# Kernel tuning notes

Hardware: AMD Instinct MI355X
Metric: run time of the kernel (lower is better)

## Reference

```python
import jax, jax.numpy as jnp
import numpy as np

NEG_INF = -1e30  # fp32-safe sentinel for masked max


def setup_inputs() -> dict:
    key = jax.random.key(0)
    ks = jax.random.split(key, 8)
    E = 65536          # num_edge
    S = 1              # neg_samples
    D = 200            # dim_in_time + dim_in_node
    H = 100            # hardcoded hidden width of src_fc/dst_fc
    T = 8              # num edge types
    C = 1              # predict_class
    scale = 1.0 / np.sqrt(D)
    return {
        "h": jax.random.normal(ks[0], (E * (S + 2), D), dtype=jnp.float32),
        "src_W": jax.random.normal(ks[1], (T, D, H), dtype=jnp.float32) * scale,
        "src_b": jax.random.normal(ks[2], (T, H), dtype=jnp.float32) * 0.01,
        "dst_W": jax.random.normal(ks[3], (T, D, H), dtype=jnp.float32) * scale,
        "dst_b": jax.random.normal(ks[4], (T, H), dtype=jnp.float32) * 0.01,
        "out_W": jax.random.normal(ks[5], (T, H, C), dtype=jnp.float32) * (1.0 / np.sqrt(H)),
        "out_b": jax.random.normal(ks[6], (T, C), dtype=jnp.float32) * 0.01,
        "poss_edgetypes": jax.random.randint(ks[7], (E * (1 + S), T), 0, 2, dtype=jnp.int32),
        "neg_samples": S,
    }


def _masked_max_pred(h_s, h_d, mask, src_W, src_b, dst_W, dst_b, out_W, out_b):
    # h_s, h_d: [N, D]; mask: [N, T] bool
    src_enc = jnp.einsum('nd,tdh->nth', h_s, src_W) + src_b      # [N, T, H]
    dst_enc = jnp.einsum('nd,tdh->nth', h_d, dst_W) + dst_b      # [N, T, H]
    hid = jax.nn.relu(src_enc + dst_enc)                          # [N, T, H]
    pred = jnp.einsum('nth,thc->ntc', hid, out_W) + out_b        # [N, T, C]
    masked = jnp.where(mask[:, :, None], pred, NEG_INF)
    best = jnp.max(masked, axis=1)                                # [N, C]
    any_valid = jnp.any(mask, axis=1, keepdims=True)
    return jnp.where(any_valid, best, 0.0)                        # zeros if no valid type


def reference(h, src_W, src_b, dst_W, dst_b, out_W, out_b, poss_edgetypes, neg_samples):
    E = h.shape[0] // (neg_samples + 2)
    h_src = h[:E]
    h_pos_dst = h[E:2 * E]
    h_neg_dst = h[2 * E:]                                         # [S*E, D], neg-major order
    mask = poss_edgetypes.astype(bool)
    pos_mask = mask[:E]
    neg_mask = mask[E:]
    pos_pred = _masked_max_pred(h_src, h_pos_dst, pos_mask,
                                src_W, src_b, dst_W, dst_b, out_W, out_b)
    h_src_tiled = jnp.tile(h_src, (neg_samples, 1))               # matches global_neg_idx = src + neg*E
    neg_pred = _masked_max_pred(h_src_tiled, h_neg_dst, neg_mask,
                                src_W, src_b, dst_W, dst_b, out_W, out_b)
    return pos_pred, neg_pred
```

## Files before the change

kernel.cpp:

```cpp
#include <hip/hip_runtime.h>
#include <stdint.h>


typedef float f32x4 __attribute__((ext_vector_type(4)));
typedef short s16x8 __attribute__((ext_vector_type(8)));

static constexpr int E_NODES = 65536;
static constexpr int D_DIM   = 200;
static constexpr int H_DIM   = 100;
static constexpr int T_TYPES = 8;
static constexpr int NPAD    = 112;
static constexpr int NT      = 7;
static constexpr int KS      = 13;
static constexpr int BK      = 128;
static constexpr int SLPT    = 4;
static constexpr int P_TILE  = 128;
static constexpr int THREADS = 256;
static constexpr int N_INT   = T_TYPES * SLPT;
static constexpr int SLAB_ELEMS = NPAD * BK;
static constexpr int XFERS_PT   = SLAB_ELEMS * 2 / 16 / THREADS;

__device__ unsigned short g_Wt[N_INT * SLAB_ELEMS];

__device__ __forceinline__ unsigned short f2bf(float f) {
  unsigned int u = __float_as_uint(f);
  u += 0x7FFFu + ((u >> 16) & 1u);
  return (unsigned short)(u >> 16);
}

__global__ void prep_weights(const float* __restrict__ srcW, const float* __restrict__ dstW) {
  int idx = blockIdx.x * blockDim.x + threadIdx.x;
  const int total = N_INT * SLAB_ELEMS;
  if (idx >= total) return;
  int j   = idx % NPAD;
  int rem = idx / NPAD;
  int kk  = rem % BK;
  int rs  = rem / BK;
  int sl  = rs & 3;
  int t   = rs >> 2;
  int k   = sl * BK + kk;
  float v = 0.0f;
  if (j < H_DIM) {
    if (k < D_DIM)            v = srcW[(t * D_DIM + k) * H_DIM + j];
    else if (k < 2 * D_DIM)   v = dstW[(t * D_DIM + (k - D_DIM)) * H_DIM + j];
  }
  int kks = kk ^ ((j & 7) << 3);
  g_Wt[(rs * NPAD + j) * BK + kks] = f2bf(v);
}

__device__ __forceinline__ void stage(int rs, unsigned short* dst, int tid) {
  const char* src = (const char*)g_Wt + (size_t)rs * SLAB_ELEMS * 2;
  char* d = (char*)dst;
#pragma unroll
  for (int i = 0; i < XFERS_PT; ++i) {
    const int off = (i * THREADS + tid) * 16;
    __builtin_amdgcn_global_load_lds(
        (const __attribute__((address_space(1))) void*)(src + off),
        (__attribute__((address_space(3))) void*)(d + off),
        16, 0, 0);
  }
}

__global__ __launch_bounds__(THREADS, 2)
void fused_pred(const float* __restrict__ h,
                const float* __restrict__ srcB, const float* __restrict__ dstB,
                const float* __restrict__ outW, const float* __restrict__ outB,
                const int* __restrict__ poss, float* __restrict__ out) {
  __shared__ __align__(16) unsigned short ldsB[2][SLAB_ELEMS];
  __shared__ __align__(16) int   ldsMask[P_TILE * T_TYPES];
  __shared__ float ldsBias[T_TYPES * NPAD];
  __shared__ float ldsOutw[T_TYPES * NPAD];
  __shared__ float ldsOutb[T_TYPES];

  const int tid  = threadIdx.x;
  const int lane = tid & 63;
  const int w    = tid >> 6;
  const int c    = lane & 15;
  const int g    = lane >> 4;

  const int l     = ((int)blockIdx.x & 7) * 128 + ((int)blockIdx.x >> 3);
  const int which = l & 1;
  const int grp   = l >> 1;
  const int P0    = which * E_NODES + grp * P_TILE;

  stage(0, ldsB[0], tid);
  __builtin_amdgcn_sched_barrier(0);

#pragma unroll
  for (int i = 0; i < 4; ++i) {
    int idx = i * THREADS + tid;
    if (idx < T_TYPES * NPAD) {
      int t = idx / NPAD, j = idx - t * NPAD;
      float bb = 0.f, ww = 0.f;
      if (j < H_DIM) {
        bb = srcB[t * H_DIM + j] + dstB[t * H_DIM + j];
        ww = outW[t * H_DIM + j];
      }
      ldsBias[idx] = bb;
      ldsOutw[idx] = ww;
    }
  }
  if (tid < T_TYPES) ldsOutb[tid] = outB[tid];
  ((int4*)ldsMask)[tid] = ((const int4*)(poss + (size_t)P0 * T_TYPES))[tid];

  s16x8 A[2][KS];
#pragma unroll
  for (int mt = 0; mt < 2; ++mt) {
    const int row = w * 32 + mt * 16 + c;
    const int p   = P0 + row;
    const float* sp = h + (size_t)(p & (E_NODES - 1)) * D_DIM;
    const float* dp = h + ((size_t)E_NODES + (size_t)p) * D_DIM;
#pragma unroll
    for (int ks = 0; ks < KS; ++ks) {
      const int k0 = ks * 32 + g * 8;
      s16x8 a = {};
      if (k0 < 2 * D_DIM) {
        const float* base = (k0 < D_DIM) ? (sp + k0) : (dp + (k0 - D_DIM));
        float4 f0 = *(const float4*)(base);
        float4 f1 = *(const float4*)(base + 4);
        a[0] = (short)f2bf(f0.x); a[1] = (short)f2bf(f0.y);
        a[2] = (short)f2bf(f0.z); a[3] = (short)f2bf(f0.w);
        a[4] = (short)f2bf(f1.x); a[5] = (short)f2bf(f1.y);
        a[6] = (short)f2bf(f1.z); a[7] = (short)f2bf(f1.w);
      }
      A[mt][ks] = a;
    }
  }

  const f32x4 ZERO4 = {0.f, 0.f, 0.f, 0.f};
  f32x4 acc[2][NT];
  float runmax[2][4];
#pragma unroll
  for (int mt = 0; mt < 2; ++mt) {
#pragma unroll
    for (int nt = 0; nt < NT; ++nt) acc[mt][nt] = ZERO4;
#pragma unroll
    for (int r = 0; r < 4; ++r) runmax[mt][r] = -1e30f;
  }

  const int swz = (c & 7) << 4;

  __syncthreads();

  for (int t = 0; t < T_TYPES; ++t) {
#pragma unroll
    for (int sl = 0; sl < SLPT; ++sl) {
      if (sl < SLPT - 1 || t < T_TYPES - 1)
        stage(t * SLPT + sl + 1, ldsB[(sl + 1) & 1], tid);
      __builtin_amdgcn_sched_barrier(0);

      const char* B = (const char*)ldsB[sl & 1];
#pragma unroll
      for (int ksl = 0; ksl < 4; ++ksl) {
        const int ksg = sl * 4 + ksl;
        if (ksg < KS) {
          const int koff = (ksl * 64 + g * 16) ^ swz;
          const s16x8 a0 = A[0][ksg];
          const s16x8 a1 = A[1][ksg];
#pragma unroll
          for (int nt = 0; nt < NT; ++nt) {
            s16x8 b = *(const s16x8*)(B + (nt * 16 + c) * 256 + koff);
            acc[0][nt] = __builtin_amdgcn_mfma_f32_16x16x32_bf16(a0, b, acc[0][nt], 0, 0, 0);
            acc[1][nt] = __builtin_amdgcn_mfma_f32_16x16x32_bf16(a1, b, acc[1][nt], 0, 0, 0);
          }
        }
      }

      if (sl == SLPT - 1) {
        float bj[NT], wj[NT];
#pragma unroll
        for (int nt = 0; nt < NT; ++nt) {
          bj[nt] = ldsBias[t * NPAD + nt * 16 + c];
          wj[nt] = ldsOutw[t * NPAD + nt * 16 + c];
        }
        const float ob = ldsOutb[t];
#pragma unroll
        for (int mt = 0; mt < 2; ++mt) {
#pragma unroll
          for (int r = 0; r < 4; ++r) {
            float v = 0.f;
#pragma unroll
            for (int nt = 0; nt < NT; ++nt)
              v += fmaxf(acc[mt][nt][r] + bj[nt], 0.f) * wj[nt];
            v += __shfl_xor(v, 1);
            v += __shfl_xor(v, 2);
            v += __shfl_xor(v, 4);
            v += __shfl_xor(v, 8);
            const float pred = v + ob;
            const int row = w * 32 + mt * 16 + g * 4 + r;
            if (ldsMask[row * T_TYPES + t] != 0)
              runmax[mt][r] = fmaxf(runmax[mt][r], pred);
          }
#pragma unroll
          for (int nt = 0; nt < NT; ++nt) acc[mt][nt] = ZERO4;
        }
      }

      __syncthreads();
    }
  }

  if (c == 0) {
#pragma unroll
    for (int mt = 0; mt < 2; ++mt)
#pragma unroll
      for (int r = 0; r < 4; ++r) {
        const int row = w * 32 + mt * 16 + g * 4 + r;
        const float v = runmax[mt][r];
        out[P0 + row] = (v > -1e29f) ? v : 0.0f;
      }
  }
}

extern "C" void kernel_launch(void* const* d_in, const int* in_sizes, int n_in,
                              void* d_out, int out_size, void* d_ws, size_t ws_size,
                              hipStream_t stream) {
  const float* h    = (const float*)d_in[0];
  const float* srcW = (const float*)d_in[1];
  const float* srcB = (const float*)d_in[2];
  const float* dstW = (const float*)d_in[3];
  const float* dstB = (const float*)d_in[4];
  const float* outW = (const float*)d_in[5];
  const float* outB = (const float*)d_in[6];
  const int*   poss = (const int*)d_in[7];
  float* out = (float*)d_out;

  const int prep_total = N_INT * SLAB_ELEMS;
  prep_weights<<<(prep_total + 255) / 256, 256, 0, stream>>>(srcW, dstW);

  const int nblocks = (2 * E_NODES) / P_TILE;
  fused_pred<<<nblocks, THREADS, 0, stream>>>(h, srcB, dstB, outW, outB, poss, out);
}
```

Before: 328.9 us.

## Load MFMA B fragments directly from global memory instead of LDS staging

Weights are repacked into a fragment-major layout so each lane can read its MFMA B operand straight from global memory (served by L2/L1), with register double-buffering across k-steps. The LDS slab ring and per-slab barriers are removed, and the block grows to 512 threads covering 256 rows. This trades LDS traffic and synchronisation for redundant per-wave global/cache reads of the weights and higher register pressure from the bb buffers.

Result: slower. 420.5 us (+27.8%).

```diff
diff --git a/kernel.cpp b/kernel.cpp
--- a/kernel.cpp
+++ b/kernel.cpp
@@ -12,15 +12,14 @@
 static constexpr int NPAD    = 112;
 static constexpr int NT      = 7;
 static constexpr int KS      = 13;
-static constexpr int BK      = 128;
-static constexpr int SLPT    = 4;
-static constexpr int P_TILE  = 128;
-static constexpr int THREADS = 256;
-static constexpr int N_INT   = T_TYPES * SLPT;
-static constexpr int SLAB_ELEMS = NPAD * BK;
-static constexpr int XFERS_PT   = SLAB_ELEMS * 2 / 16 / THREADS;
-
-__device__ unsigned short g_Wt[N_INT * SLAB_ELEMS];
+static constexpr int P_TILE  = 256;
+static constexpr int THREADS = 512;
+static constexpr int REC_B   = 1024;
+static constexpr int KSG_B   = NT * REC_B;
+static constexpr int T_B     = KS * KSG_B;
+static constexpr int WT_ELEMS = T_TYPES * KS * NT * 512;
+
+__device__ unsigned short g_Wt[WT_ELEMS];
 
 __device__ __forceinline__ unsigned short f2bf(float f) {
   unsigned int u = __float_as_uint(f);
@@ -30,35 +29,22 @@
 
 __global__ void prep_weights(const float* __restrict__ srcW, const float* __restrict__ dstW) {
   int idx = blockIdx.x * blockDim.x + threadIdx.x;
-  const int total = N_INT * SLAB_ELEMS;
-  if (idx >= total) return;
-  int j   = idx % NPAD;
-  int rem = idx / NPAD;
-  int kk  = rem % BK;
-  int rs  = rem / BK;
-  int sl  = rs & 3;
-  int t   = rs >> 2;
-  int k   = sl * BK + kk;
+  if (idx >= WT_ELEMS) return;
+  int e   = idx & 7;
+  int l   = (idx >> 3) & 63;
+  int rec = idx >> 9;
+  int nt  = rec % 7;
+  int r2  = rec / 7;
+  int ksg = r2 % 13;
+  int t   = r2 / 13;
+  int j   = nt * 16 + (l & 15);
+  int k   = ksg * 32 + ((l >> 4) << 3) + e;
   float v = 0.0f;
   if (j < H_DIM) {
-    if (k < D_DIM)            v = srcW[(t * D_DIM + k) * H_DIM + j];
-    else if (k < 2 * D_DIM)   v = dstW[(t * D_DIM + (k - D_DIM)) * H_DIM + j];
-  }
-  int kks = kk ^ ((j & 7) << 3);
-  g_Wt[(rs * NPAD + j) * BK + kks] = f2bf(v);
-}
-
-__device__ __forceinline__ void stage(int rs, unsigned short* dst, int tid) {
-  const char* src = (const char*)g_Wt + (size_t)rs * SLAB_ELEMS * 2;
-  char* d = (char*)dst;
-#pragma unroll
-  for (int i = 0; i < XFERS_PT; ++i) {
-    const int off = (i * THREADS + tid) * 16;
-    __builtin_amdgcn_global_load_lds(
-        (const __attribute__((address_space(1))) void*)(src + off),
-        (__attribute__((address_space(3))) void*)(d + off),
-        16, 0, 0);
-  }
+    if (k < D_DIM)          v = srcW[(t * D_DIM + k) * H_DIM + j];
+    else if (k < 2 * D_DIM) v = dstW[(t * D_DIM + (k - D_DIM)) * H_DIM + j];
+  }
+  g_Wt[idx] = f2bf(v);
 }
 
 __global__ __launch_bounds__(THREADS, 2)
@@ -66,8 +52,7 @@
                 const float* __restrict__ srcB, const float* __restrict__ dstB,
                 const float* __restrict__ outW, const float* __restrict__ outB,
                 const int* __restrict__ poss, float* __restrict__ out) {
-  __shared__ __align__(16) unsigned short ldsB[2][SLAB_ELEMS];
-  __shared__ __align__(16) int   ldsMask[P_TILE * T_TYPES];
+  __shared__ __align__(16) int ldsMask[P_TILE * T_TYPES];
   __shared__ float ldsBias[T_TYPES * NPAD];
   __shared__ float ldsOutw[T_TYPES * NPAD];
   __shared__ float ldsOutb[T_TYPES];
@@ -78,16 +63,13 @@
   const int c    = lane & 15;
   const int g    = lane >> 4;
 
-  const int l     = ((int)blockIdx.x & 7) * 128 + ((int)blockIdx.x >> 3);
+  const int l     = ((int)blockIdx.x & 7) * 64 + ((int)blockIdx.x >> 3);
   const int which = l & 1;
   const int grp   = l >> 1;
   const int P0    = which * E_NODES + grp * P_TILE;
 
-  stage(0, ldsB[0], tid);
-  __builtin_amdgcn_sched_barrier(0);
-
-#pragma unroll
-  for (int i = 0; i < 4; ++i) {
+#pragma unroll
+  for (int i = 0; i < 2; ++i) {
     int idx = i * THREADS + tid;
     if (idx < T_TYPES * NPAD) {
       int t = idx / NPAD, j = idx - t * NPAD;
@@ -138,66 +120,64 @@
     for (int r = 0; r < 4; ++r) runmax[mt][r] = -1e30f;
   }
 
-  const int swz = (c & 7) << 4;
-
   __syncthreads();
 
   for (int t = 0; t < T_TYPES; ++t) {
-#pragma unroll
-    for (int sl = 0; sl < SLPT; ++sl) {
-      if (sl < SLPT - 1 || t < T_TYPES - 1)
-        stage(t * SLPT + sl + 1, ldsB[(sl + 1) & 1], tid);
-      __builtin_amdgcn_sched_barrier(0);
-
-      const char* B = (const char*)ldsB[sl & 1];
-#pragma unroll
-      for (int ksl = 0; ksl < 4; ++ksl) {
-        const int ksg = sl * 4 + ksl;
-        if (ksg < KS) {
-          const int koff = (ksl * 64 + g * 16) ^ swz;
-          const s16x8 a0 = A[0][ksg];
-          const s16x8 a1 = A[1][ksg];
-#pragma unroll
-          for (int nt = 0; nt < NT; ++nt) {
-            s16x8 b = *(const s16x8*)(B + (nt * 16 + c) * 256 + koff);
-            acc[0][nt] = __builtin_amdgcn_mfma_f32_16x16x32_bf16(a0, b, acc[0][nt], 0, 0, 0);
-            acc[1][nt] = __builtin_amdgcn_mfma_f32_16x16x32_bf16(a1, b, acc[1][nt], 0, 0, 0);
-          }
+    const char* bt = (const char*)g_Wt + (size_t)t * T_B + lane * 16;
+
+    s16x8 bb[2][NT];
+#pragma unroll
+    for (int nt = 0; nt < NT; ++nt)
+      bb[0][nt] = *(const s16x8*)(bt + 0 * KSG_B + nt * REC_B);
+
+#pragma unroll
+    for (int ksg = 0; ksg < KS; ++ksg) {
+      const int cur = ksg & 1;
+      if (ksg < KS - 1) {
+#pragma unroll
+        for (int nt = 0; nt < NT; ++nt)
+          bb[cur ^ 1][nt] = *(const s16x8*)(bt + (ksg + 1) * KSG_B + nt * REC_B);
+      }
+      const s16x8 a0 = A[0][ksg];
+      const s16x8 a1 = A[1][ksg];
+#pragma unroll
+      for (int nt = 0; nt < NT; ++nt) {
+        acc[0][nt] = __builtin_amdgcn_mfma_f32_16x16x32_bf16(a0, bb[cur][nt], acc[0][nt], 0, 0, 0);
+        acc[1][nt] = __builtin_amdgcn_mfma_f32_16x16x32_bf16(a1, bb[cur][nt], acc[1][nt], 0, 0, 0);
+      }
+    }
+
+    {
+      float bj[NT], wj[NT];
+#pragma unroll
+      for (int nt = 0; nt < NT; ++nt) {
+        bj[nt] = ldsBias[t * NPAD + nt * 16 + c];
+        wj[nt] = ldsOutw[t * NPAD + nt * 16 + c];
+      }
+      const float ob = ldsOutb[t];
+#pragma unroll
+      for (int mt = 0; mt < 2; ++mt) {
+#pragma unroll
+        for (int r = 0; r < 4; ++r) {
+          float v = 0.f;
+#pragma unroll
+          for (int nt = 0; nt < NT; ++nt)
+            v += fmaxf(acc[mt][nt][r] + bj[nt], 0.f) * wj[nt];
+          v += __shfl_xor(v, 1);
+          v += __shfl_xor(v, 2);
+          v += __shfl_xor(v, 4);
+          v += __shfl_xor(v, 8);
+          const float pred = v + ob;
+          const int row = w * 32 + mt * 16 + g * 4 + r;
+          if (ldsMask[row * T_TYPES + t] != 0)
+            runmax[mt][r] = fmaxf(runmax[mt][r], pred);
         }
-      }
-
-      if (sl == SLPT - 1) {
-        float bj[NT], wj[NT];
-#pragma unroll
-        for (int nt = 0; nt < NT; ++nt) {
-          bj[nt] = ldsBias[t * NPAD + nt * 16 + c];
-          wj[nt] = ldsOutw[t * NPAD + nt * 16 + c];
-        }
-        const float ob = ldsOutb[t];
-#pragma unroll
-        for (int mt = 0; mt < 2; ++mt) {
-#pragma unroll
-          for (int r = 0; r < 4; ++r) {
-            float v = 0.f;
-#pragma unroll
-            for (int nt = 0; nt < NT; ++nt)
-              v += fmaxf(acc[mt][nt][r] + bj[nt], 0.f) * wj[nt];
-            v += __shfl_xor(v, 1);
-            v += __shfl_xor(v, 2);
-            v += __shfl_xor(v, 4);
-            v += __shfl_xor(v, 8);
-            const float pred = v + ob;
-            const int row = w * 32 + mt * 16 + g * 4 + r;
-            if (ldsMask[row * T_TYPES + t] != 0)
-              runmax[mt][r] = fmaxf(runmax[mt][r], pred);
-          }
-#pragma unroll
-          for (int nt = 0; nt < NT; ++nt) acc[mt][nt] = ZERO4;
-        }
-      }
-
-      __syncthreads();
-    }
+#pragma unroll
+        for (int nt = 0; nt < NT; ++nt) acc[mt][nt] = ZERO4;
+      }
+    }
+
+    __syncthreads();
   }
 
   if (c == 0) {
@@ -225,8 +205,7 @@
   const int*   poss = (const int*)d_in[7];
   float* out = (float*)d_out;
 
-  const int prep_total = N_INT * SLAB_ELEMS;
-  prep_weights<<<(prep_total + 255) / 256, 256, 0, stream>>>(srcW, dstW);
+  prep_weights<<<(WT_ELEMS + 255) / 256, 256, 0, stream>>>(srcW, dstW);
 
   const int nblocks = (2 * E_NODES) / P_TILE;
   fused_pred<<<nblocks, THREADS, 0, stream>>>(h, srcB, dstB, outW, outB, poss, out);
```
